# Kernel optimization log

Measured on AMD Instinct MI355X. Metric: run time of the kernel, lower is better.

Reference implementation:

```python
import jax, jax.numpy as jnp
import numpy as np

N, NPG, BS = 32000, 1000, 32
E, H, L, R, K = 512000, 128, 3, 8, 64


def setup_inputs() -> dict:
    key = jax.random.key(0)
    ks = jax.random.split(key, 16)
    sc = 0.05
    x = jax.random.normal(ks[0], (N, H), jnp.float32)
    W_rel = jax.random.normal(ks[1], (L, R, H, H), jnp.float32) * sc
    W_self = jax.random.normal(ks[2], (L, H, H), jnp.float32) * sc
    rel_table = jax.random.normal(ks[3], (R, H), jnp.float32)
    Zn = jax.random.normal(ks[4], (K, H), jnp.float32) * sc
    proj_W = jax.random.normal(ks[5], (L * H, H), jnp.float32) * sc
    proj_b = jnp.zeros((H,), jnp.float32)
    fc_W = jax.random.normal(ks[6], (2 * L * H + 2 * H, 1), jnp.float32) * sc
    fc_b = jnp.zeros((1,), jnp.float32)
    rep_seq = jax.random.normal(ks[7], (BS, H), jnp.float32)
    src = jax.random.randint(ks[8], (E,), 0, N, jnp.int32)
    dst = jax.random.randint(ks[9], (E,), 0, N, jnp.int32)
    etype = jax.random.randint(ks[10], (E,), 0, R, jnp.int32)
    graph_id = (jnp.arange(N, dtype=jnp.int32) // NPG).astype(jnp.int32)
    head_ids = (jnp.arange(BS, dtype=jnp.int32) * NPG)           # node with id==1 per subgraph
    tail_ids = (jnp.arange(BS, dtype=jnp.int32) * NPG + 1)       # node with id==2 per subgraph
    rel_labels = jax.random.randint(ks[11], (BS,), 0, R, jnp.int32)
    return dict(x=x, W_rel=W_rel, W_self=W_self, rel_table=rel_table, Zn=Zn,
                proj_W=proj_W, proj_b=proj_b, fc_W=fc_W, fc_b=fc_b, rep_seq=rep_seq,
                src=src, dst=dst, etype=etype, graph_id=graph_id,
                head_ids=head_ids, tail_ids=tail_ids, rel_labels=rel_labels)


def reference(x, W_rel, W_self, rel_table, Zn, proj_W, proj_b, fc_W, fc_b, rep_seq,
              src, dst, etype, graph_id, head_ids, tail_ids, rel_labels):
    n, h_dim = x.shape
    bs = head_ids.shape[0]
    # RGCN message passing: aggregate src features per (dst, rel), then per-rel linear.
    seg = dst.astype(jnp.int32) * R + etype.astype(jnp.int32)  # [E]
    h = x
    reprs = []
    for l in range(L):
        agg = jax.ops.segment_sum(h[src], seg, num_segments=n * R)  # [N*R, H]
        agg = agg.reshape(n, R, h_dim)
        msg = jnp.einsum('nri,rio->no', agg, W_rel[l])
        h = jax.nn.relu(msg + h @ W_self[l])
        reprs.append(h)
    repr_ = jnp.stack(reprs, axis=1)  # [N, L, H]
    # mean_nodes pooling per subgraph
    counts = jax.ops.segment_sum(jnp.ones((n,), x.dtype), graph_id, num_segments=bs)
    g_mean = jax.ops.segment_sum(repr_, graph_id, num_segments=bs) / counts[:, None, None]
    g_out = jax.nn.leaky_relu(g_mean.reshape(bs, L * h_dim) @ proj_W + proj_b)  # [bs, H]
    # head/tail gathers
    head_flat = repr_[head_ids].reshape(bs, L * h_dim)
    tail_flat = repr_[tail_ids].reshape(bs, L * h_dim)
    rel_embs = rel_table[rel_labels]  # [bs, H]
    h_out = head_flat @ proj_W + proj_b
    t_out = tail_flat @ proj_W + proj_b
    # community view: cluster assignment (softmax) then summary (sigmoid)
    s1 = jax.nn.sigmoid(jax.nn.softmax(h_out @ Zn.T, axis=-1) @ Zn)
    s2 = jax.nn.sigmoid(jax.nn.softmax(t_out @ Zn.T, axis=-1) @ Zn)
    s = s1 * s2
    # view attention aggregation over [subgraph, sequence, community] views
    views = jnp.stack([g_out, rep_seq, s], axis=1)  # [bs, 3, H]
    att = jax.nn.softmax(jnp.sum(rel_embs[:, None, :] * views, axis=-1), axis=-1)  # [bs, 3]
    view_aggr = jnp.sum(att[:, :, None] * views, axis=1)  # [bs, H]
    # positive triplet scoring
    g_rep = jnp.concatenate([head_flat, tail_flat, rel_embs, view_aggr], axis=1)
    out_pos = g_rep @ fc_W + fc_b  # [bs, 1]
    return out_pos
```

## Files before the change

### kernel.cpp

```cpp
#include <hip/hip_runtime.h>

#define N_NODES 32000
#define NPG     1000
#define BSZ     32
#define NEDGE   512000
#define H       128
#define NL      3
#define NR      8
#define NKK     1152
#define NBIN2   262144

typedef __attribute__((ext_vector_type(8))) short short8;
typedef __attribute__((ext_vector_type(4))) float float4v;

__device__ __forceinline__ float bf2f(unsigned short u) {
  union { unsigned int i; float f; } v;
  v.i = ((unsigned int)u) << 16;
  return v.f;
}
__device__ __forceinline__ unsigned short f2bf(float f) {
  union { float f; unsigned int i; } v;
  v.f = f;
  unsigned int x = v.i;
  return (unsigned short)((x + 0x7FFFu + ((x >> 16) & 1u)) >> 16);
}

__device__ __forceinline__ void gl_lds16(const void* g, void* l) {
  __builtin_amdgcn_global_load_lds((__attribute__((address_space(1))) void*)g,
                                   (__attribute__((address_space(3))) void*)l,
                                   16, 0, 0);
}

__global__ __launch_bounds__(256) void k_prep(
    const float* __restrict__ x, const float* __restrict__ W_rel,
    const float* __restrict__ W_self, const int* __restrict__ dst,
    const int* __restrict__ etype, const int* __restrict__ graph_id,
    unsigned short* __restrict__ hb, unsigned short* __restrict__ Bt,
    int* __restrict__ cnt, int* __restrict__ gcount)
{
  const int b = blockIdx.x, t = threadIdx.x;
  if (b < 4000) {
    const size_t i = ((size_t)b * 256 + t) * 4;
    float4 v = *(const float4*)(x + i);
    ushort4 u = { f2bf(v.x), f2bf(v.y), f2bf(v.z), f2bf(v.w) };
    *(ushort4*)(hb + i) = u;
  } else if (b < 5728) {
    const int g = (b - 4000) * 256 + t;
    const int l = g / (H * NKK);
    const int rem = g - l * (H * NKK);
    const int o = rem / NKK;
    const int kk = rem - o * NKK;
    float v = (kk < 1024)
        ? W_rel[(((size_t)l * NR + (kk >> 7)) * H + (kk & 127)) * H + o]
        : W_self[((size_t)l * H + (kk - 1024)) * H + o];
    Bt[g] = f2bf(v);
  } else if (b < 7728) {
    const int e = (b - 5728) * 256 + t;
    atomicAdd(&cnt[dst[e] * 8 + etype[e]], 1);
  } else {
    __shared__ int hist[BSZ];
    if (t < BSZ) hist[t] = 0;
    __syncthreads();
    const int n = (b - 7728) * 256 + t;
    if (n < N_NODES) atomicAdd(&hist[graph_id[n]], 1);
    __syncthreads();
    if (t < BSZ) { int v = hist[t]; if (v) atomicAdd(&gcount[t], v); }
  }
}

__global__ __launch_bounds__(256) void k_scanA(const int* __restrict__ cnt,
                                               int* __restrict__ bsum) {
  __shared__ int red[256];
  const int t = threadIdx.x;
  int4 v = *(const int4*)(cnt + blockIdx.x * 1024 + t * 4);
  red[t] = v.x + v.y + v.z + v.w;
  __syncthreads();
  for (int off = 128; off > 0; off >>= 1) {
    if (t < off) red[t] += red[t + off];
    __syncthreads();
  }
  if (t == 0) bsum[blockIdx.x] = red[0];
}

__global__ __launch_bounds__(256) void k_scanC(const int* __restrict__ cnt,
                                               const int* __restrict__ bsum,
                                               int* __restrict__ row_ptr2,
                                               int* __restrict__ cursor) {
  __shared__ int ts[256], bsx[256];
  const int t = threadIdx.x;
  const int base = blockIdx.x * 1024 + t * 4;
  int4 v = *(const int4*)(cnt + base);
  const int s = v.x + v.y + v.z + v.w;
  ts[t]  = s;
  bsx[t] = bsum[t];
  __syncthreads();
  for (int off = 1; off < 256; off <<= 1) {
    int a = (t >= off) ? ts[t - off]  : 0;
    int c = (t >= off) ? bsx[t - off] : 0;
    __syncthreads();
    ts[t] += a; bsx[t] += c;
    __syncthreads();
  }
  const int boff = (blockIdx.x == 0) ? 0 : bsx[blockIdx.x - 1];
  int ex = ts[t] - s + boff;
  int4 w = { ex, ex + v.x, ex + v.x + v.y, ex + v.x + v.y + v.z };
  *(int4*)(row_ptr2 + base) = w;
  *(int4*)(cursor + base) = w;
}

__global__ void k_fill(const int* __restrict__ src, const int* __restrict__ dst,
                       const int* __restrict__ etype, int* __restrict__ cursor,
                       int* __restrict__ edge_off) {
  int e = blockIdx.x * blockDim.x + threadIdx.x;
  if (e < NEDGE) {
    int p = atomicAdd(&cursor[dst[e] * 8 + etype[e]], 1);
    edge_off[p] = src[e];
  }
}

__global__ __launch_bounds__(256) void k_agg(
    const unsigned short* __restrict__ Hin,
    const int* __restrict__ row_ptr2,
    const int* __restrict__ edge_off,
    unsigned short* __restrict__ A)
{
  const int tid = threadIdx.x;
  const int j = tid >> 5;
  const int li = tid & 31;
  const int n = blockIdx.x;
  const unsigned int* Hu = (const unsigned int*)Hin;
  const int b = row_ptr2[n * 8 + j];
  const int e = row_ptr2[n * 8 + j + 1];
  float a0 = 0.f, a1 = 0.f, a2 = 0.f, a3 = 0.f;
#define ACCW(xx, yy) { \
    a0 += bf2f((unsigned short)((xx) & 0xffff)); \
    a1 += bf2f((unsigned short)((xx) >> 16));    \
    a2 += bf2f((unsigned short)((yy) & 0xffff)); \
    a3 += bf2f((unsigned short)((yy) >> 16)); }
  for (int k = b; k < e; k += 4) {
    const bool v1 = (k + 1) < e, v2 = (k + 2) < e, v3 = (k + 3) < e;
    const int o0 = edge_off[k];
    const int o1 = edge_off[v1 ? k + 1 : k];
    const int o2 = edge_off[v2 ? k + 2 : k];
    const int o3 = edge_off[v3 ? k + 3 : k];
    uint2 u0 = *(const uint2*)(Hu + (size_t)o0 * 64 + li * 2);
    uint2 u1 = *(const uint2*)(Hu + (size_t)o1 * 64 + li * 2);
    uint2 u2 = *(const uint2*)(Hu + (size_t)o2 * 64 + li * 2);
    uint2 u3 = *(const uint2*)(Hu + (size_t)o3 * 64 + li * 2);
    ACCW(u0.x, u0.y)
    ACCW(v1 ? u1.x : 0u, v1 ? u1.y : 0u)
    ACCW(v2 ? u2.x : 0u, v2 ? u2.y : 0u)
    ACCW(v3 ? u3.x : 0u, v3 ? u3.y : 0u)
  }
#undef ACCW
  ushort4 w4 = { f2bf(a0), f2bf(a1), f2bf(a2), f2bf(a3) };
  *(ushort4*)(A + (size_t)n * NKK + j * H + li * 4) = w4;
  if (j == 0) {
    uint2 u = *(const uint2*)(Hu + (size_t)n * 64 + li * 2);
    *(uint2*)(A + (size_t)n * NKK + 1024 + li * 4) = u;
  }
}

__global__ __launch_bounds__(256, 3) void k_gemmA(
    const unsigned short* __restrict__ Ag,
    const unsigned short* __restrict__ Bg,
    unsigned short* __restrict__ Hout)
{
  __shared__ __align__(16) unsigned short pool[24576];
  const int tid = threadIdx.x;
  const int w = tid >> 6, lane = tid & 63;
  const int l15 = lane & 15, quad = lane >> 4;
  const int m0 = blockIdx.x * 64;
  const int rbase = (w & 1) * 32;
  const int cbase = (w >> 1) * 64;

  float4v acc[2][4];
  #pragma unroll
  for (int i = 0; i < 2; ++i)
    #pragma unroll
    for (int jj = 0; jj < 4; ++jj) acc[i][jj] = (float4v){0.f, 0.f, 0.f, 0.f};

  {
    #pragma unroll
    for (int rep = 0; rep < 2; ++rep) {
      const int g = rep * 256 + tid, row = g >> 3, c = g & 7;
      gl_lds16(Ag + (size_t)(m0 + row) * NKK + ((c ^ (row & 7)) * 8), pool + (size_t)g * 8);
    }
    #pragma unroll
    for (int rep = 0; rep < 4; ++rep) {
      const int g = rep * 256 + tid, row = g >> 3, c = g & 7;
      gl_lds16(Bg + (size_t)row * NKK + ((c ^ (row & 7)) * 8), pool + 4096 + (size_t)g * 8);
    }
  }
  __syncthreads();

  #pragma unroll 2
  for (int kt = 0; kt < 18; ++kt) {
    const int cur = kt & 1;
    const unsigned short* ac = pool + (cur ? 12288 : 0);
    const unsigned short* bc = pool + (cur ? 16384 : 4096);
    if (kt < 17) {
      unsigned short* an = pool + (cur ? 0 : 12288);
      unsigned short* bn = pool + (cur ? 4096 : 16384);
      const int kb = (kt + 1) * 64;
      #pragma unroll
      for (int rep = 0; rep < 2; ++rep) {
        const int g = rep * 256 + tid, row = g >> 3, c = g & 7;
        gl_lds16(Ag + (size_t)(m0 + row) * NKK + kb + ((c ^ (row & 7)) * 8), an + (size_t)g * 8);
      }
      #pragma unroll
      for (int rep = 0; rep < 4; ++rep) {
        const int g = rep * 256 + tid, row = g >> 3, c = g & 7;
        gl_lds16(Bg + (size_t)row * NKK + kb + ((c ^ (row & 7)) * 8), bn + (size_t)g * 8);
      }
    }
    #pragma unroll
    for (int s = 0; s < 2; ++s) {
      const int c = s * 4 + quad;
      short8 af[2], bfv[4];
      #pragma unroll
      for (int i = 0; i < 2; ++i) {
        const int row = rbase + i * 16 + l15;
        af[i] = *(const short8*)(ac + row * 64 + ((c ^ (row & 7)) * 8));
      }
      #pragma unroll
      for (int jj = 0; jj < 4; ++jj) {
        const int orow = cbase + jj * 16 + l15;
        bfv[jj] = *(const short8*)(bc + orow * 64 + ((c ^ (orow & 7)) * 8));
      }
      #pragma unroll
      for (int i = 0; i < 2; ++i)
        #pragma unroll
        for (int jj = 0; jj < 4; ++jj)
          acc[i][jj] = __builtin_amdgcn_mfma_f32_16x16x32_bf16(af[i], bfv[jj], acc[i][jj], 0, 0, 0);
    }
    __syncthreads();
  }

  #pragma unroll
  for (int i = 0; i < 2; ++i)
    #pragma unroll
    for (int jj = 0; jj < 4; ++jj)
      #pragma unroll
      for (int r = 0; r < 4; ++r) {
        const int row = rbase + i * 16 + quad * 4 + r;
        const int col = cbase + jj * 16 + l15;
        pool[row * 136 + col] = f2bf(fmaxf(acc[i][jj][r], 0.f));
      }
  __syncthreads();
  #pragma unroll
  for (int rep = 0; rep < 4; ++rep) {
    const int g = rep * 256 + tid;
    const int row = g >> 4, c = g & 15;
    *(uint4*)(Hout + (size_t)(m0 + row) * H + c * 8) = *(const uint4*)(pool + row * 136 + c * 8);
  }
}

__global__ void k_gmean(const unsigned short* __restrict__ hb, float* __restrict__ gmean)
{
  const int g = blockIdx.x, l = blockIdx.y, c = blockIdx.z, t = threadIdx.x;
  const unsigned short* base =
      hb + ((size_t)(l + 1) * N_NODES + (size_t)g * NPG + (size_t)c * (NPG / 8)) * H + t * 2;
  float sx = 0.f, sy = 0.f;
  for (int i = 0; i < 125; ++i) {
    unsigned int u = *(const unsigned int*)(base + (size_t)i * H);
    sx += bf2f((unsigned short)(u & 0xffff));
    sy += bf2f((unsigned short)(u >> 16));
  }
  float* gp = gmean + (size_t)g * (NL * H) + l * H + t * 2;
  atomicAdd(gp, sx);
  atomicAdd(gp + 1, sy);
}

__global__ __launch_bounds__(128) void k_final(
    const unsigned short* __restrict__ hb, const float* __restrict__ gmean,
    const int* __restrict__ gcount,
    const float* __restrict__ rel_tb, const float* __restrict__ Zn,
    const float* __restrict__ projW, const float* __restrict__ projB,
    const float* __restrict__ fcW, const float* __restrict__ fcB,
    const float* __restrict__ repSeq,
    const int* __restrict__ head_ids, const int* __restrict__ tail_ids,
    const int* __restrict__ rel_lab, float* __restrict__ out)
{
  const int b = blockIdx.x;
  const int o = threadIdx.x;
  __shared__ float gm[384], hf[384], tf[384];
  __shared__ float go[128], ho[128], t_o[128], re[128], rs[128], sv[128];
  __shared__ float lg[128], pr[128], red[128], att[3];

  const int hid = head_ids[b], tlid = tail_ids[b], rl = rel_lab[b];
  const float cinv = 1.f / (float)gcount[b];
  #pragma unroll
  for (int l = 0; l < NL; ++l) {
    gm[l * H + o] = gmean[(size_t)b * (NL * H) + l * H + o] * cinv;
    hf[l * H + o] = bf2f(hb[((size_t)(l + 1) * N_NODES + hid) * H + o]);
    tf[l * H + o] = bf2f(hb[((size_t)(l + 1) * N_NODES + tlid) * H + o]);
  }
  re[o] = rel_tb[rl * H + o];
  rs[o] = repSeq[b * H + o];
  __syncthreads();

  float pb = projB[o];
  float sg = pb, sh = pb, st = pb;
  for (int i = 0; i < NL * H; ++i) {
    float wv = projW[i * H + o];
    sg = fmaf(gm[i], wv, sg);
    sh = fmaf(hf[i], wv, sh);
    st = fmaf(tf[i], wv, st);
  }
  go[o] = (sg > 0.f) ? sg : 0.01f * sg;
  ho[o] = sh;
  t_o[o] = st;
  __syncthreads();

  {
    const int k = o & 63;
    const float* v = (o < 64) ? ho : t_o;
    float s = 0.f;
    for (int i = 0; i < H; ++i) s = fmaf(v[i], Zn[k * H + i], s);
    lg[o] = s;
  }
  __syncthreads();
  if (o < 2) {
    float* l0 = &lg[o * 64];
    float* p0 = &pr[o * 64];
    float mx = l0[0];
    for (int k = 1; k < 64; ++k) mx = fmaxf(mx, l0[k]);
    float sum = 0.f;
    for (int k = 0; k < 64; ++k) { float e = __expf(l0[k] - mx); p0[k] = e; sum += e; }
    float inv = 1.f / sum;
    for (int k = 0; k < 64; ++k) p0[k] *= inv;
  }
  __syncthreads();
  {
    float s1 = 0.f, s2 = 0.f;
    for (int k = 0; k < 64; ++k) {
      float z = Zn[k * H + o];
      s1 = fmaf(pr[k], z, s1);
      s2 = fmaf(pr[64 + k], z, s2);
    }
    s1 = 1.f / (1.f + __expf(-s1));
    s2 = 1.f / (1.f + __expf(-s2));
    sv[o] = s1 * s2;
  }
  __syncthreads();
  if (o == 0) {
    float d0 = 0.f, d1 = 0.f, d2 = 0.f;
    for (int i = 0; i < H; ++i) { d0 += re[i] * go[i]; d1 += re[i] * rs[i]; d2 += re[i] * sv[i]; }
    float mx = fmaxf(d0, fmaxf(d1, d2));
    float e0 = __expf(d0 - mx), e1 = __expf(d1 - mx), e2 = __expf(d2 - mx);
    float inv = 1.f / (e0 + e1 + e2);
    att[0] = e0 * inv; att[1] = e1 * inv; att[2] = e2 * inv;
  }
  __syncthreads();
  float va = att[0] * go[o] + att[1] * rs[o] + att[2] * sv[o];

  float p = 0.f;
  p = fmaf(hf[o],       fcW[o],       p);
  p = fmaf(hf[128 + o], fcW[128 + o], p);
  p = fmaf(hf[256 + o], fcW[256 + o], p);
  p = fmaf(tf[o],       fcW[384 + o], p);
  p = fmaf(tf[128 + o], fcW[512 + o], p);
  p = fmaf(tf[256 + o], fcW[640 + o], p);
  p = fmaf(re[o],       fcW[768 + o], p);
  p = fmaf(va,          fcW[896 + o], p);
  red[o] = p;
  __syncthreads();
  if (o == 0) {
    float s = 0.f;
    for (int i = 0; i < 128; ++i) s += red[i];
    out[b] = s + fcB[0];
  }
}

extern "C" void kernel_launch(void* const* d_in, const int* in_sizes, int n_in,
                              void* d_out, int out_size, void* d_ws, size_t ws_size,
                              hipStream_t stream) {
  const float* x        = (const float*)d_in[0];
  const float* W_rel    = (const float*)d_in[1];
  const float* W_self   = (const float*)d_in[2];
  const float* rel_tb   = (const float*)d_in[3];
  const float* Zn       = (const float*)d_in[4];
  const float* proj_W   = (const float*)d_in[5];
  const float* proj_b   = (const float*)d_in[6];
  const float* fc_W     = (const float*)d_in[7];
  const float* fc_b     = (const float*)d_in[8];
  const float* rep_seq  = (const float*)d_in[9];
  const int* src      = (const int*)d_in[10];
  const int* dst      = (const int*)d_in[11];
  const int* etype    = (const int*)d_in[12];
  const int* graph_id = (const int*)d_in[13];
  const int* head_ids = (const int*)d_in[14];
  const int* tail_ids = (const int*)d_in[15];
  const int* rel_lab  = (const int*)d_in[16];
  float* out = (float*)d_out;

  char* w = (char*)d_ws;
  unsigned short* A   = (unsigned short*)w; w += (size_t)N_NODES * NKK * 2;
  unsigned short* hb  = (unsigned short*)w; w += (size_t)(NL + 1) * N_NODES * H * 2;
  unsigned short* Bt2 = (unsigned short*)w; w += (size_t)NL * H * NKK * 2;
  int* row_ptr2 = (int*)w;  w += (size_t)(NBIN2 + 8) * 4;
  int* cursor   = (int*)w;  w += (size_t)NBIN2 * 4;
  int* edge_off = (int*)w;  w += (size_t)NEDGE * 4;
  int* bsum     = (int*)w;  w += (size_t)256 * 4;
  char* z = w;
  int* cnt     = (int*)w;   w += (size_t)NBIN2 * 4;
  int* gcount  = (int*)w;   w += (size_t)32 * 4;
  float* gmean = (float*)w; w += (size_t)BSZ * NL * H * 4;
  size_t zbytes = (size_t)(w - z);

  hipMemsetAsync(z, 0, zbytes, stream);
  k_prep <<<7853, 256, 0, stream>>>(x, W_rel, W_self, dst, etype, graph_id, hb, Bt2, cnt, gcount);
  k_scanA<<<NBIN2 / 1024, 256, 0, stream>>>(cnt, bsum);
  k_scanC<<<NBIN2 / 1024, 256, 0, stream>>>(cnt, bsum, row_ptr2, cursor);
  k_fill <<<NEDGE / 256, 256, 0, stream>>>(src, dst, etype, cursor, edge_off);

  for (int l = 0; l < NL; ++l) {
    const unsigned short* hp = hb + (size_t)l * N_NODES * H;
    unsigned short* hn = hb + (size_t)(l + 1) * N_NODES * H;
    k_agg  <<<N_NODES, 256, 0, stream>>>(hp, row_ptr2, edge_off, A);
    k_gemmA<<<N_NODES / 64, 256, 0, stream>>>(A, Bt2 + (size_t)l * H * NKK, hn);
  }
  k_gmean<<<dim3(BSZ, NL, 8), 64, 0, stream>>>(hb, gmean);
  k_final<<<BSZ, H, 0, stream>>>(hb, gmean, gcount, rel_tb, Zn, proj_W, proj_b, fc_W, fc_b,
                                 rep_seq, head_ids, tail_ids, rel_lab, out);
  (void)in_sizes; (void)n_in; (void)out_size; (void)ws_size;
}
```

Before: 343.4 us.

## Fuse graph-mean into GEMM epilogue, read self features directly, widen aggregation loads

The aggregation kernel now gathers 16-byte rows with two half-warps that take alternating edges and are combined with a shuffle. It no longer copies the self features into the A matrix, so A shrinks to 1024 columns and the GEMM streams its last K tile straight from the previous layer's features. The separate graph-mean kernel is removed, and the per-graph column sums are computed in the GEMM epilogue from the LDS tile and added with atomics. This cuts global traffic and one launch, at the cost of more atomics and extra epilogue work in the GEMM.

```diff
diff --git a/kernel.cpp b/kernel.cpp
--- a/kernel.cpp
+++ b/kernel.cpp
@@ -8,6 +8,7 @@
 #define NL      3
 #define NR      8
 #define NKK     1152
+#define NKA     1024
 #define NBIN2   262144
 
 typedef __attribute__((ext_vector_type(8))) short short8;
@@ -125,46 +126,55 @@
     unsigned short* __restrict__ A)
 {
   const int tid = threadIdx.x;
-  const int j = tid >> 5;
+  const int j  = tid >> 5;
   const int li = tid & 31;
-  const int n = blockIdx.x;
-  const unsigned int* Hu = (const unsigned int*)Hin;
+  const int p  = li >> 4;
+  const int q  = li & 15;
+  const int n  = blockIdx.x;
+  const uint4* H4 = (const uint4*)Hin;
   const int b = row_ptr2[n * 8 + j];
   const int e = row_ptr2[n * 8 + j + 1];
-  float a0 = 0.f, a1 = 0.f, a2 = 0.f, a3 = 0.f;
-#define ACCW(xx, yy) { \
-    a0 += bf2f((unsigned short)((xx) & 0xffff)); \
-    a1 += bf2f((unsigned short)((xx) >> 16));    \
-    a2 += bf2f((unsigned short)((yy) & 0xffff)); \
-    a3 += bf2f((unsigned short)((yy) >> 16)); }
-  for (int k = b; k < e; k += 4) {
-    const bool v1 = (k + 1) < e, v2 = (k + 2) < e, v3 = (k + 3) < e;
+  float acc[8] = {0.f, 0.f, 0.f, 0.f, 0.f, 0.f, 0.f, 0.f};
+#define ACC8(u, ok) { \
+    const unsigned int xx = (ok) ? (u).x : 0u, yy = (ok) ? (u).y : 0u; \
+    const unsigned int zz = (ok) ? (u).z : 0u, ww = (ok) ? (u).w : 0u; \
+    acc[0] += bf2f((unsigned short)(xx & 0xffff)); \
+    acc[1] += bf2f((unsigned short)(xx >> 16));    \
+    acc[2] += bf2f((unsigned short)(yy & 0xffff)); \
+    acc[3] += bf2f((unsigned short)(yy >> 16));    \
+    acc[4] += bf2f((unsigned short)(zz & 0xffff)); \
+    acc[5] += bf2f((unsigned short)(zz >> 16));    \
+    acc[6] += bf2f((unsigned short)(ww & 0xffff)); \
+    acc[7] += bf2f((unsigned short)(ww >> 16)); }
+  for (int k = b + p; k < e; k += 4) {
+    const int k1 = k + 2;
+    const bool v1 = k1 < e;
     const int o0 = edge_off[k];
-    const int o1 = edge_off[v1 ? k + 1 : k];
-    const int o2 = edge_off[v2 ? k + 2 : k];
-    const int o3 = edge_off[v3 ? k + 3 : k];
-    uint2 u0 = *(const uint2*)(Hu + (size_t)o0 * 64 + li * 2);
-    uint2 u1 = *(const uint2*)(Hu + (size_t)o1 * 64 + li * 2);
-    uint2 u2 = *(const uint2*)(Hu + (size_t)o2 * 64 + li * 2);
-    uint2 u3 = *(const uint2*)(Hu + (size_t)o3 * 64 + li * 2);
-    ACCW(u0.x, u0.y)
-    ACCW(v1 ? u1.x : 0u, v1 ? u1.y : 0u)
-    ACCW(v2 ? u2.x : 0u, v2 ? u2.y : 0u)
-    ACCW(v3 ? u3.x : 0u, v3 ? u3.y : 0u)
-  }
-#undef ACCW
-  ushort4 w4 = { f2bf(a0), f2bf(a1), f2bf(a2), f2bf(a3) };
-  *(ushort4*)(A + (size_t)n * NKK + j * H + li * 4) = w4;
-  if (j == 0) {
-    uint2 u = *(const uint2*)(Hu + (size_t)n * 64 + li * 2);
-    *(uint2*)(A + (size_t)n * NKK + 1024 + li * 4) = u;
+    const int o1 = edge_off[v1 ? k1 : k];
+    uint4 u0 = H4[(size_t)o0 * 16 + q];
+    uint4 u1 = H4[(size_t)o1 * 16 + q];
+    ACC8(u0, true)
+    ACC8(u1, v1)
+  }
+#undef ACC8
+  #pragma unroll
+  for (int i = 0; i < 8; ++i) acc[i] += __shfl_xor(acc[i], 16);
+  if (p == 0) {
+    uint4 w;
+    w.x = (unsigned int)f2bf(acc[0]) | ((unsigned int)f2bf(acc[1]) << 16);
+    w.y = (unsigned int)f2bf(acc[2]) | ((unsigned int)f2bf(acc[3]) << 16);
+    w.z = (unsigned int)f2bf(acc[4]) | ((unsigned int)f2bf(acc[5]) << 16);
+    w.w = (unsigned int)f2bf(acc[6]) | ((unsigned int)f2bf(acc[7]) << 16);
+    *(uint4*)(A + (size_t)n * NKA + j * H + q * 8) = w;
   }
 }
 
 __global__ __launch_bounds__(256, 3) void k_gemmA(
     const unsigned short* __restrict__ Ag,
     const unsigned short* __restrict__ Bg,
-    unsigned short* __restrict__ Hout)
+    const unsigned short* __restrict__ Hin,
+    unsigned short* __restrict__ Hout,
+    float* __restrict__ gmean, int layer)
 {
   __shared__ __align__(16) unsigned short pool[24576];
   const int tid = threadIdx.x;
@@ -180,18 +190,26 @@
     #pragma unroll
     for (int jj = 0; jj < 4; ++jj) acc[i][jj] = (float4v){0.f, 0.f, 0.f, 0.f};
 
-  {
+  auto stageA = [&](unsigned short* dstL, const int kb) {
     #pragma unroll
     for (int rep = 0; rep < 2; ++rep) {
       const int g = rep * 256 + tid, row = g >> 3, c = g & 7;
-      gl_lds16(Ag + (size_t)(m0 + row) * NKK + ((c ^ (row & 7)) * 8), pool + (size_t)g * 8);
-    }
+      const unsigned short* srcp = (kb < NKA)
+          ? Ag  + (size_t)(m0 + row) * NKA + kb + ((c ^ (row & 7)) * 8)
+          : Hin + (size_t)(m0 + row) * H + (kb - NKA) + ((c ^ (row & 7)) * 8);
+      gl_lds16(srcp, dstL + (size_t)g * 8);
+    }
+  };
+  auto stageB = [&](unsigned short* dstL, const int kb) {
     #pragma unroll
     for (int rep = 0; rep < 4; ++rep) {
       const int g = rep * 256 + tid, row = g >> 3, c = g & 7;
-      gl_lds16(Bg + (size_t)row * NKK + ((c ^ (row & 7)) * 8), pool + 4096 + (size_t)g * 8);
-    }
-  }
+      gl_lds16(Bg + (size_t)row * NKK + kb + ((c ^ (row & 7)) * 8), dstL + (size_t)g * 8);
+    }
+  };
+
+  stageA(pool, 0);
+  stageB(pool + 4096, 0);
   __syncthreads();
 
   #pragma unroll 2
@@ -200,19 +218,9 @@
     const unsigned short* ac = pool + (cur ? 12288 : 0);
     const unsigned short* bc = pool + (cur ? 16384 : 4096);
     if (kt < 17) {
-      unsigned short* an = pool + (cur ? 0 : 12288);
-      unsigned short* bn = pool + (cur ? 4096 : 16384);
       const int kb = (kt + 1) * 64;
-      #pragma unroll
-      for (int rep = 0; rep < 2; ++rep) {
-        const int g = rep * 256 + tid, row = g >> 3, c = g & 7;
-        gl_lds16(Ag + (size_t)(m0 + row) * NKK + kb + ((c ^ (row & 7)) * 8), an + (size_t)g * 8);
-      }
-      #pragma unroll
-      for (int rep = 0; rep < 4; ++rep) {
-        const int g = rep * 256 + tid, row = g >> 3, c = g & 7;
-        gl_lds16(Bg + (size_t)row * NKK + kb + ((c ^ (row & 7)) * 8), bn + (size_t)g * 8);
-      }
+      stageA(pool + (cur ? 0 : 12288), kb);
+      stageB(pool + (cur ? 4096 : 16384), kb);
     }
     #pragma unroll
     for (int s = 0; s < 2; ++s) {
@@ -254,22 +262,20 @@
     const int row = g >> 4, c = g & 15;
     *(uint4*)(Hout + (size_t)(m0 + row) * H + c * 8) = *(const uint4*)(pool + row * 136 + c * 8);
   }
-}
-
-__global__ void k_gmean(const unsigned short* __restrict__ hb, float* __restrict__ gmean)
-{
-  const int g = blockIdx.x, l = blockIdx.y, c = blockIdx.z, t = threadIdx.x;
-  const unsigned short* base =
-      hb + ((size_t)(l + 1) * N_NODES + (size_t)g * NPG + (size_t)c * (NPG / 8)) * H + t * 2;
-  float sx = 0.f, sy = 0.f;
-  for (int i = 0; i < 125; ++i) {
-    unsigned int u = *(const unsigned int*)(base + (size_t)i * H);
-    sx += bf2f((unsigned short)(u & 0xffff));
-    sy += bf2f((unsigned short)(u >> 16));
-  }
-  float* gp = gmean + (size_t)g * (NL * H) + l * H + t * 2;
-  atomicAdd(gp, sx);
-  atomicAdd(gp + 1, sy);
+
+  const int g0 = m0 / NPG;
+  const int bnd = (g0 + 1) * NPG - m0;
+  if (tid < H) {
+    float s0 = 0.f, s1 = 0.f;
+    #pragma unroll 8
+    for (int r2 = 0; r2 < 64; ++r2) {
+      float v = bf2f(pool[r2 * 136 + tid]);
+      if (r2 < bnd) s0 += v; else s1 += v;
+    }
+    atomicAdd(&gmean[(size_t)g0 * (NL * H) + layer * H + tid], s0);
+    if (bnd < 64)
+      atomicAdd(&gmean[(size_t)(g0 + 1) * (NL * H) + layer * H + tid], s1);
+  }
 }
 
 __global__ __launch_bounds__(128) void k_final(
@@ -396,7 +402,7 @@
   float* out = (float*)d_out;
 
   char* w = (char*)d_ws;
-  unsigned short* A   = (unsigned short*)w; w += (size_t)N_NODES * NKK * 2;
+  unsigned short* A   = (unsigned short*)w; w += (size_t)N_NODES * NKA * 2;
   unsigned short* hb  = (unsigned short*)w; w += (size_t)(NL + 1) * N_NODES * H * 2;
   unsigned short* Bt2 = (unsigned short*)w; w += (size_t)NL * H * NKK * 2;
   int* row_ptr2 = (int*)w;  w += (size_t)(NBIN2 + 8) * 4;
@@ -419,9 +425,8 @@
     const unsigned short* hp = hb + (size_t)l * N_NODES * H;
     unsigned short* hn = hb + (size_t)(l + 1) * N_NODES * H;
     k_agg  <<<N_NODES, 256, 0, stream>>>(hp, row_ptr2, edge_off, A);
-    k_gemmA<<<N_NODES / 64, 256, 0, stream>>>(A, Bt2 + (size_t)l * H * NKK, hn);
-  }
-  k_gmean<<<dim3(BSZ, NL, 8), 64, 0, stream>>>(hb, gmean);
+    k_gemmA<<<N_NODES / 64, 256, 0, stream>>>(A, Bt2 + (size_t)l * H * NKK, hp, hn, gmean, l);
+  }
   k_final<<<BSZ, H, 0, stream>>>(hb, gmean, gcount, rel_tb, Zn, proj_W, proj_b, fc_W, fc_b,
                                  rep_seq, head_ids, tail_ids, rel_lab, out);
   (void)in_sizes; (void)n_in; (void)out_size; (void)ws_size;
```

New measurement: 333.3 us. -2.9%, faster.
